# Kernel optimization log

Measured on AMD Instinct MI355X. Metric: run time of the kernel, lower is better.

Reference implementation:

```python
import jax, jax.numpy as jnp
import numpy as np

K = 3  # kernel_size

def setup_inputs() -> dict:
    key = jax.random.key(0)
    ks = jax.random.split(key, 7)
    B, C, H, W = 4, 128, 128, 128
    MID = int(C * 0.2)  # 25
    return {
        "x":  jax.random.normal(ks[0], (B, C, H, W), dtype=jnp.float32),
        "Ws": jax.random.normal(ks[1], (K * K, C), dtype=jnp.float32) * 0.1,
        "bs": jax.random.normal(ks[2], (K * K,), dtype=jnp.float32) * 0.1,
        "W1": jax.random.normal(ks[3], (MID, C), dtype=jnp.float32) * 0.1,
        "b1": jax.random.normal(ks[4], (MID,), dtype=jnp.float32) * 0.1,
        "W2": jax.random.normal(ks[5], (C * K * K, MID), dtype=jnp.float32) * 0.1,
        "b2": jax.random.normal(ks[6], (C * K * K,), dtype=jnp.float32) * 0.1,
    }

def reference(x, Ws, bs, W1, b1, W2, b2):
    b, c, h, w = x.shape
    k = K
    # channel branch: global avg pool -> 1x1 conv -> relu -> 1x1 conv -> sigmoid
    xm = x.mean(axis=(2, 3))                                   # [b, c]
    hid = jax.nn.relu(xm @ W1.T + b1)                          # [b, mid]
    channel_filter = jax.nn.sigmoid(hid @ W2.T + b2)           # [b, c*k*k]
    channel_filter = channel_filter.reshape(b, c, k * k, 1, 1)
    # spatial branch: 1x1 conv C -> k*k, sigmoid
    spatial_filter = jax.nn.sigmoid(
        jnp.einsum('bchw,oc->bohw', x, Ws) + bs[None, :, None, None]
    ).reshape(b, 1, k * k, h, w)
    filt = spatial_filter * channel_filter                     # [b, c, k*k, h, w]
    # unfold (k=3, pad=1, stride=1, dilation=1): stack 9 shifted views
    xp = jnp.pad(x, ((0, 0), (0, 0), (1, 1), (1, 1)))
    patches = jnp.stack(
        [xp[:, :, i:i + h, j:j + w] for i in range(k) for j in range(k)],
        axis=2,
    )  # [b, c, k*k, h, w] — matches nn.Unfold's (c, k*k) ordering
    return (patches * filt).sum(axis=2)                        # [b, c, h, w]
```

## Files before the change

### kernel.cpp

```cpp
#include <hip/hip_runtime.h>

#define B 4
#define C 128
#define H 128
#define W 128
#define HW (H * W)
#define KK 9
#define MID 25

#define SPATIAL_BLKS (HW / 64)

#define WS_XM 0
#define WS_CH 1024
#define WS_S  8192

__global__ __launch_bounds__(256) void k_ms(
    const float* __restrict__ x, const float* __restrict__ Ws,
    const float* __restrict__ bs, float* __restrict__ xm,
    float* __restrict__ S)
{
    __shared__ float red[3 * KK * 64];
    const int b = blockIdx.y;

    if (blockIdx.x >= SPATIAL_BLKS) {
        const int c = blockIdx.x - SPATIAL_BLKS;
        const float4* plane = (const float4*)(x + ((size_t)b * C + c) * HW);
        float s = 0.0f;
#pragma unroll
        for (int i = 0; i < 16; ++i) {
            float4 v = plane[i * 256 + threadIdx.x];
            s += (v.x + v.y) + (v.z + v.w);
        }
#pragma unroll
        for (int off = 32; off > 0; off >>= 1) s += __shfl_down(s, off, 64);
        if ((threadIdx.x & 63) == 0) red[threadIdx.x >> 6] = s;
        __syncthreads();
        if (threadIdx.x == 0)
            xm[b * C + c] = ((red[0] + red[1]) + (red[2] + red[3])) * (1.0f / HW);
        return;
    }

    const int lane = threadIdx.x & 63;
    const int wave = threadIdx.x >> 6;
    const int p = blockIdx.x * 64 + lane;
    const float* xb = x + (size_t)b * C * HW + p;

    float acc[KK];
#pragma unroll
    for (int k = 0; k < KK; ++k) acc[k] = (wave == 0) ? bs[k] : 0.0f;

    const int cbase = wave * 32;
#pragma unroll
    for (int i = 0; i < 32; ++i) {
        const int c = cbase + i;
        float v = xb[(size_t)c * HW];
#pragma unroll
        for (int k = 0; k < KK; ++k)
            acc[k] = fmaf(v, Ws[k * C + c], acc[k]);
    }

    if (wave > 0) {
#pragma unroll
        for (int k = 0; k < KK; ++k)
            red[((wave - 1) * KK + k) * 64 + lane] = acc[k];
    }
    __syncthreads();
    if (wave == 0) {
#pragma unroll
        for (int k = 0; k < KK; ++k) {
            float a = acc[k] + red[(0 * KK + k) * 64 + lane]
                             + red[(1 * KK + k) * 64 + lane]
                             + red[(2 * KK + k) * 64 + lane];
            S[((size_t)(b * KK + k)) * HW + p] = 1.0f / (1.0f + __expf(-a));
        }
    }
}

__global__ __launch_bounds__(256) void k_mlp(
    const float* __restrict__ xm, const float* __restrict__ W1,
    const float* __restrict__ b1, const float* __restrict__ W2,
    const float* __restrict__ b2, float* __restrict__ ch)
{
    __shared__ float xmean[B * C];
    __shared__ float hid[B * MID];
    const int tid = threadIdx.x;

    for (int i = tid; i < B * C; i += 256) xmean[i] = xm[i];
    __syncthreads();

    if (tid < B * MID) {
        const int b = tid / MID, m = tid % MID;
        float a = b1[m];
#pragma unroll 8
        for (int c = 0; c < C; ++c)
            a = fmaf(xmean[b * C + c], W1[m * C + c], a);
        hid[tid] = fmaxf(a, 0.0f);
    }
    __syncthreads();

    const int idx = blockIdx.x * 256 + tid;
    const int b = idx / (C * KK);
    const int o = idx % (C * KK);
    float a = b2[o];
#pragma unroll
    for (int m = 0; m < MID; ++m)
        a = fmaf(hid[b * MID + m], W2[o * MID + m], a);
    ch[idx] = 1.0f / (1.0f + __expf(-a));
}

__global__ __launch_bounds__(256) void k_conv(
    const float* __restrict__ x, const float* __restrict__ S,
    const float* __restrict__ ch, float* __restrict__ out)
{
    const int tid = threadIdx.x;
    const int b = blockIdx.y;
    const int p0 = (blockIdx.x * 256 + tid) * 4;
    const int h = p0 >> 7;
    const int w0 = p0 & (W - 1);

    float4 sv[KK];
    const float* Sb = S + (size_t)b * KK * HW + p0;
#pragma unroll
    for (int k = 0; k < KK; ++k) {
        const int di = k / 3 - 1, dj = k % 3 - 1;
        const int hh = h + di;
        float4 s4 = *(const float4*)(Sb + (size_t)k * HW);
        if (hh < 0 || hh >= H) s4 = make_float4(0.f, 0.f, 0.f, 0.f);
        if (dj == -1 && w0 == 0)     s4.x = 0.f;
        if (dj == +1 && w0 == W - 4) s4.w = 0.f;
        sv[k] = s4;
    }

    const int r0 = max(h - 1, 0), r2 = min(h + 1, H - 1);
    const int rowoff[3] = { r0 * W + w0, h * W + w0, r2 * W + w0 };
    const int loff = (w0 > 0) ? -1 : 0;
    const int roff = (w0 < W - 4) ? 4 : 0;

    const int c0 = blockIdx.z * (C / 16);
    const float* xb = x + (size_t)b * C * HW;
    const float* chb = ch + b * C * KK;
    float* ob = out + (size_t)b * C * HW + p0;

    for (int c = c0; c < c0 + C / 16; ++c) {
        const float* xc = xb + (size_t)c * HW;
        float4 Cx[3];
        float  Lw[3], Rx[3];
#pragma unroll
        for (int r = 0; r < 3; ++r) {
            const float* bp = xc + rowoff[r];
            Cx[r] = *(const float4*)bp;
            Lw[r] = bp[loff];
            Rx[r] = bp[roff];
        }
        float4 a = make_float4(0.f, 0.f, 0.f, 0.f);
#pragma unroll
        for (int k = 0; k < KK; ++k) {
            const int r = k / 3, dj = k % 3 - 1;
            float4 t;
            if (dj == -1)     t = make_float4(Lw[r], Cx[r].x, Cx[r].y, Cx[r].z);
            else if (dj == 0) t = Cx[r];
            else              t = make_float4(Cx[r].y, Cx[r].z, Cx[r].w, Rx[r]);
            const float cf = chb[c * KK + k];
            a.x = fmaf(t.x, sv[k].x * cf, a.x);
            a.y = fmaf(t.y, sv[k].y * cf, a.y);
            a.z = fmaf(t.z, sv[k].z * cf, a.z);
            a.w = fmaf(t.w, sv[k].w * cf, a.w);
        }
        *(float4*)(ob + (size_t)c * HW) = a;
    }
}

extern "C" void kernel_launch(void* const* d_in, const int* in_sizes, int n_in,
                              void* d_out, int out_size, void* d_ws, size_t ws_size,
                              hipStream_t stream) {
    (void)in_sizes; (void)n_in; (void)out_size; (void)ws_size;
    const float* x  = (const float*)d_in[0];
    const float* Ws = (const float*)d_in[1];
    const float* bs = (const float*)d_in[2];
    const float* W1 = (const float*)d_in[3];
    const float* b1 = (const float*)d_in[4];
    const float* W2 = (const float*)d_in[5];
    const float* b2 = (const float*)d_in[6];
    float* out = (float*)d_out;
    float* ws  = (float*)d_ws;

    float* xm = ws + WS_XM;
    float* ch = ws + WS_CH;
    float* S  = ws + WS_S;

    k_ms<<<dim3(SPATIAL_BLKS + C, B), 256, 0, stream>>>(x, Ws, bs, xm, S);
    k_mlp<<<18, 256, 0, stream>>>(xm, W1, b1, W2, b2, ch);
    k_conv<<<dim3(HW / 1024, B, 16), 256, 0, stream>>>(x, S, ch, out);
}
```

Before: 127.0 us.

## Fuse channel mean into spatial pass via per-block partial sums

Removes the separate channel-mean blocks that re-read all of x. The spatial conv pass now also computes per-block channel partial sums with wave shuffles and writes them to workspace. The MLP kernel then reduces 256 partials per (batch, channel) before the first layer. The conv grid is also reordered so channel-group blocks sharing the same pixels launch adjacently, which may improve L2 reuse of S and neighbouring x rows. This costs extra shuffles in the spatial loop and a serial reduction in the single-wave-heavy MLP kernel.

```diff
diff --git a/kernel.cpp b/kernel.cpp
--- a/kernel.cpp
+++ b/kernel.cpp
@@ -10,36 +10,17 @@
 
 #define SPATIAL_BLKS (HW / 64)
 
-#define WS_XM 0
-#define WS_CH 1024
-#define WS_S  8192
+#define WS_CH   1024
+#define WS_S    8192
+#define WS_PART 600064
 
 __global__ __launch_bounds__(256) void k_ms(
     const float* __restrict__ x, const float* __restrict__ Ws,
-    const float* __restrict__ bs, float* __restrict__ xm,
+    const float* __restrict__ bs, float* __restrict__ part,
     float* __restrict__ S)
 {
     __shared__ float red[3 * KK * 64];
     const int b = blockIdx.y;
-
-    if (blockIdx.x >= SPATIAL_BLKS) {
-        const int c = blockIdx.x - SPATIAL_BLKS;
-        const float4* plane = (const float4*)(x + ((size_t)b * C + c) * HW);
-        float s = 0.0f;
-#pragma unroll
-        for (int i = 0; i < 16; ++i) {
-            float4 v = plane[i * 256 + threadIdx.x];
-            s += (v.x + v.y) + (v.z + v.w);
-        }
-#pragma unroll
-        for (int off = 32; off > 0; off >>= 1) s += __shfl_down(s, off, 64);
-        if ((threadIdx.x & 63) == 0) red[threadIdx.x >> 6] = s;
-        __syncthreads();
-        if (threadIdx.x == 0)
-            xm[b * C + c] = ((red[0] + red[1]) + (red[2] + red[3])) * (1.0f / HW);
-        return;
-    }
-
     const int lane = threadIdx.x & 63;
     const int wave = threadIdx.x >> 6;
     const int p = blockIdx.x * 64 + lane;
@@ -50,6 +31,7 @@
     for (int k = 0; k < KK; ++k) acc[k] = (wave == 0) ? bs[k] : 0.0f;
 
     const int cbase = wave * 32;
+    float msum = 0.0f;
 #pragma unroll
     for (int i = 0; i < 32; ++i) {
         const int c = cbase + i;
@@ -57,7 +39,13 @@
 #pragma unroll
         for (int k = 0; k < KK; ++k)
             acc[k] = fmaf(v, Ws[k * C + c], acc[k]);
+        float s = v;
+#pragma unroll
+        for (int m = 1; m <= 32; m <<= 1) s += __shfl_xor(s, m, 64);
+        msum = (lane == i) ? s : msum;
     }
+    if (lane < 32)
+        part[((size_t)b * SPATIAL_BLKS + blockIdx.x) * C + cbase + lane] = msum;
 
     if (wave > 0) {
 #pragma unroll
@@ -77,7 +65,7 @@
 }
 
 __global__ __launch_bounds__(256) void k_mlp(
-    const float* __restrict__ xm, const float* __restrict__ W1,
+    const float* __restrict__ part, const float* __restrict__ W1,
     const float* __restrict__ b1, const float* __restrict__ W2,
     const float* __restrict__ b2, float* __restrict__ ch)
 {
@@ -85,7 +73,15 @@
     __shared__ float hid[B * MID];
     const int tid = threadIdx.x;
 
-    for (int i = tid; i < B * C; i += 256) xmean[i] = xm[i];
+    for (int i = tid; i < B * C; i += 256) {
+        const int b = i >> 7, c = i & (C - 1);
+        const float* pp = part + (size_t)b * SPATIAL_BLKS * C + c;
+        float s = 0.0f;
+#pragma unroll 8
+        for (int blk = 0; blk < SPATIAL_BLKS; ++blk)
+            s += pp[(size_t)blk * C];
+        xmean[i] = s * (1.0f / HW);
+    }
     __syncthreads();
 
     if (tid < B * MID) {
@@ -114,7 +110,7 @@
 {
     const int tid = threadIdx.x;
     const int b = blockIdx.y;
-    const int p0 = (blockIdx.x * 256 + tid) * 4;
+    const int p0 = (blockIdx.z * 256 + tid) * 4;
     const int h = p0 >> 7;
     const int w0 = p0 & (W - 1);
 
@@ -136,7 +132,7 @@
     const int loff = (w0 > 0) ? -1 : 0;
     const int roff = (w0 < W - 4) ? 4 : 0;
 
-    const int c0 = blockIdx.z * (C / 16);
+    const int c0 = blockIdx.x * (C / 16);
     const float* xb = x + (size_t)b * C * HW;
     const float* chb = ch + b * C * KK;
     float* ob = out + (size_t)b * C * HW + p0;
@@ -184,11 +180,11 @@
     float* out = (float*)d_out;
     float* ws  = (float*)d_ws;
 
-    float* xm = ws + WS_XM;
-    float* ch = ws + WS_CH;
-    float* S  = ws + WS_S;
+    float* ch   = ws + WS_CH;
+    float* S    = ws + WS_S;
+    float* part = ws + WS_PART;
 
-    k_ms<<<dim3(SPATIAL_BLKS + C, B), 256, 0, stream>>>(x, Ws, bs, xm, S);
-    k_mlp<<<18, 256, 0, stream>>>(xm, W1, b1, W2, b2, ch);
-    k_conv<<<dim3(HW / 1024, B, 16), 256, 0, stream>>>(x, S, ch, out);
+    k_ms<<<dim3(SPATIAL_BLKS, B), 256, 0, stream>>>(x, Ws, bs, part, S);
+    k_mlp<<<18, 256, 0, stream>>>(part, W1, b1, W2, b2, ch);
+    k_conv<<<dim3(16, B, HW / 1024), 256, 0, stream>>>(x, S, ch, out);
 }
```

New measurement: 154.2 us. +21.4%, slower.
